# Optimization experiments

Measured on AMD Instinct MI355X. Metric: run time of the kernel, lower is better.

Reference implementation:

```python
import jax, jax.numpy as jnp
import numpy as np

D = 256      # input_dim (object feature dim)
H = 256      # hidden_dim
N0 = 4096    # nodes in frame 0
N1 = 4096    # nodes in frame 1
E = 131072   # edges
MP_ITER = 3
LN_EPS = 1e-5


def _glorot(k, shape):
    return jax.random.normal(k, shape, jnp.float32) * (1.0 / np.sqrt(shape[0]))


def setup_inputs() -> dict:
    key = jax.random.key(0)
    ks = jax.random.split(key, 20)
    z = lambda n: jnp.zeros((n,), jnp.float32)
    o = lambda n: jnp.ones((n,), jnp.float32)
    return {
        'node0': jax.random.normal(ks[0], (N0, D), jnp.float32),
        'node1': jax.random.normal(ks[1], (N1, D), jnp.float32),
        'row': jax.random.randint(ks[2], (E,), 0, N0, jnp.int32),
        'col': jax.random.randint(ks[3], (E,), 0, N1, jnp.int32),
        # edge_mlp: Linear(2D,H) ReLU Linear(H,H) LN ReLU Linear(H,H)
        'e_w1': _glorot(ks[4], (2 * D, H)), 'e_b1': z(H),
        'e_w2': _glorot(ks[5], (H, H)),     'e_b2': z(H),
        'e_g': o(H), 'e_be': z(H),
        'e_w3': _glorot(ks[6], (H, H)),     'e_b3': z(H),
        # node_mlp: Linear(H+D,H) ReLU Linear(H,H) LN ReLU Linear(H,D)
        'n_w1': _glorot(ks[7], (H + D, H)), 'n_b1': z(H),
        'n_w2': _glorot(ks[8], (H, H)),     'n_b2': z(H),
        'n_g': o(H), 'n_be': z(H),
        'n_w3': _glorot(ks[9], (H, D)),     'n_b3': z(D),
        # edge_predictor: Linear(2D,H) ReLU Linear(H,1)
        'p_w1': _glorot(ks[10], (2 * D, H)), 'p_b1': z(H),
        'p_w2': _glorot(ks[11], (H, 1)),     'p_b2': z(1),
    }


def _ln(x, g, b):
    mu = jnp.mean(x, axis=-1, keepdims=True)
    var = jnp.mean(jnp.square(x - mu), axis=-1, keepdims=True)
    return (x - mu) * jax.lax.rsqrt(var + LN_EPS) * g + b


def reference(node0, node1, row, col,
              e_w1, e_b1, e_w2, e_b2, e_g, e_be, e_w3, e_b3,
              n_w1, n_b1, n_w2, n_b2, n_g, n_be, n_w3, n_b3,
              p_w1, p_b1, p_w2, p_b2):
    def edge_mlp(x):
        h = jax.nn.relu(x @ e_w1 + e_b1)
        h = _ln(h @ e_w2 + e_b2, e_g, e_be)
        return jax.nn.relu(h) @ e_w3 + e_b3

    def node_mlp(x):
        h = jax.nn.relu(x @ n_w1 + n_b1)
        h = _ln(h @ n_w2 + n_b2, n_g, n_be)
        return jax.nn.relu(h) @ n_w3 + n_b3

    for _ in range(MP_ITER):
        # gather -> edge MLP -> scatter-add -> node MLP (+ residual)
        e_in = jnp.concatenate([node0[row], node1[col]], axis=1)  # [E, 2D]
        edge_attr = edge_mlp(e_in)                                 # [E, H]
        agg = jax.ops.segment_sum(edge_attr, row, num_segments=node0.shape[0])  # [N0, H]
        node0 = node_mlp(jnp.concatenate([node0, agg], axis=1)) + node0

    pred_in = jnp.concatenate([node0[row], node1[col]], axis=1)   # [E, 2D]
    h = jax.nn.relu(pred_in @ p_w1 + p_b1)
    edge_preds = jax.nn.sigmoid(h @ p_w2 + p_b2)                   # [E, 1]
    return edge_preds
```

## Files before the change

kernel.cpp:

```cpp
#include <hip/hip_runtime.h>
#include <hip/hip_bf16.h>

#define NN0 4096
#define NEDGE 131072
#define NMP 3

typedef __attribute__((ext_vector_type(8))) short bf16x8;
typedef __attribute__((ext_vector_type(4))) float f32x4;

__device__ __forceinline__ unsigned short f2b(float v) {
  __hip_bfloat16 h = __float2bfloat16(v);
  return __builtin_bit_cast(unsigned short, h);
}

__device__ __forceinline__ float b2f(short s) {
  return __builtin_bit_cast(float, ((unsigned)(unsigned short)s) << 16);
}

__device__ __forceinline__ void gload_lds16(const void* g, void* l) {
  __builtin_amdgcn_global_load_lds(
      (const __attribute__((address_space(1))) void*)g,
      (__attribute__((address_space(3))) void*)l, 16, 0, 0);
}

#define MFMA(a, b, c) __builtin_amdgcn_mfma_f32_16x16x32_bf16((a), (b), (c), 0, 0, 0)

__device__ __forceinline__ void wfrag_body(const float* __restrict__ src,
                                           unsigned short* __restrict__ dst,
                                           int t, int C, int lgnkt) {
  const int j = t & 7;
  const int l = (t >> 3) & 63;
  const int rest = t >> 9;
  const int kt = rest & ((1 << lgnkt) - 1);
  const int ct = rest >> lgnkt;
  const int r = l & 15, q = l >> 4;
  const int k = (kt << 5) + (q << 3) + j;
  const int c = (ct << 4) + r;
  dst[t] = f2b(src[k * C + c]);
}

__global__ void prep_kernel(
    const float* e1, const float* e2, const float* e3,
    const float* n1, const float* n2, const float* n3, const float* p1,
    unsigned short* We1, unsigned short* We2, unsigned short* We3,
    unsigned short* Wn1, unsigned short* Wn2, unsigned short* Wn3,
    unsigned short* Wp1,
    const float* __restrict__ node0, const float* __restrict__ node1,
    unsigned short* __restrict__ n0b, float* __restrict__ n0f,
    unsigned short* __restrict__ n1b,
    const int* __restrict__ rowi, int* __restrict__ counts) {
  const int b = blockIdx.x;
  const int tid = threadIdx.x;
  if (b < 512)       wfrag_body(e1, We1, (b - 0) * 256 + tid, 256, 4);
  else if (b < 768)  wfrag_body(e2, We2, (b - 512) * 256 + tid, 256, 3);
  else if (b < 1024) wfrag_body(e3, We3, (b - 768) * 256 + tid, 256, 3);
  else if (b < 1536) wfrag_body(n1, Wn1, (b - 1024) * 256 + tid, 256, 4);
  else if (b < 1792) wfrag_body(n2, Wn2, (b - 1536) * 256 + tid, 256, 3);
  else if (b < 2048) wfrag_body(n3, Wn3, (b - 1792) * 256 + tid, 256, 3);
  else if (b < 2560) wfrag_body(p1, Wp1, (b - 2048) * 256 + tid, 256, 4);
  else {
    const int t = (b - 2560) * 256 + tid;
    const float a = node0[t], v = node1[t];
    n0b[t] = f2b(a);
    n0f[t] = a;
    n1b[t] = f2b(v);
    if (t < NEDGE) atomicAdd(&counts[rowi[t]], 1);
  }
}

__global__ void scan_kernel(const int* __restrict__ counts, int* __restrict__ pos) {
  __shared__ int part[256];
  const int t = threadIdx.x;
  const int base = t << 4;
  int local[16];
  int s = 0;
  #pragma unroll
  for (int i = 0; i < 16; ++i) { local[i] = s; s += counts[base + i]; }
  part[t] = s;
  __syncthreads();
  int val = s;
  #pragma unroll
  for (int off = 1; off < 256; off <<= 1) {
    const int add = (t >= off) ? part[t - off] : 0;
    __syncthreads();
    val += add;
    part[t] = val;
    __syncthreads();
  }
  const int excl = val - s;
  #pragma unroll
  for (int i = 0; i < 16; ++i) pos[base + i] = excl + local[i];
}

__global__ void fill_kernel(const int* __restrict__ rowi, int* __restrict__ pos,
                            int* __restrict__ perm) {
  const int e = blockIdx.x * 256 + threadIdx.x;
  if (e < NEDGE) {
    const int slot = atomicAdd(&pos[rowi[e]], 1);
    perm[slot] = e;
  }
}

__global__ __launch_bounds__(256, 2) void pre_gemm_kernel(
    const unsigned short* __restrict__ n0bA, const unsigned short* __restrict__ n1b,
    const unsigned short* __restrict__ We1, const unsigned short* __restrict__ Wp1,
    const float* __restrict__ e_b1,
    unsigned short* __restrict__ P0, unsigned short* __restrict__ P1,
    unsigned short* __restrict__ Pp1)
{
  __shared__ unsigned short smem[32 * 256];
  const int b = blockIdx.x;
  const int grp = b >> 7, mb = b & 127;
  const unsigned short* A;
  const unsigned short* W;
  int ktoff;
  const float* bias;
  unsigned short* out;
  if (grp == 0)      { A = n0bA; W = We1; ktoff = 0; bias = e_b1;    out = P0;  }
  else if (grp == 1) { A = n1b;  W = We1; ktoff = 8; bias = nullptr; out = P1;  }
  else               { A = n1b;  W = Wp1; ktoff = 8; bias = nullptr; out = Pp1; }

  const int tid = (int)threadIdx.x;
  const int ww = tid >> 6, l = tid & 63, r = l & 15, q = l >> 4;
  const int c0 = ww << 6;
  const int swz = (r & 7) << 4;

  #pragma unroll
  for (int s = 0; s < 4; ++s) {
    const int rp = (ww << 3) + (s << 1);
    const int row = rp + (l >> 5);
    const int g = (l & 31) ^ (row & 7);
    gload_lds16(A + (mb * 32 + row) * 256 + g * 8, &smem[rp * 256]);
  }
  __syncthreads();

  f32x4 acc[2][4];
  #pragma unroll
  for (int mt = 0; mt < 2; ++mt)
    #pragma unroll
    for (int nt = 0; nt < 4; ++nt)
      acc[mt][nt] = f32x4{0.f, 0.f, 0.f, 0.f};

  for (int ks = 0; ks < 8; ++ks) {
    bf16x8 a[2];
    #pragma unroll
    for (int mt = 0; mt < 2; ++mt)
      a[mt] = *(const bf16x8*)((const char*)smem + ((mt << 4) + r) * 512 +
                               (((ks << 6) | (q << 4)) ^ swz));
    #pragma unroll
    for (int nt = 0; nt < 4; ++nt) {
      bf16x8 bfr = *(const bf16x8*)(W + ((((ww << 2) + nt) << 4) + ktoff + ks) * 512 + (l << 3));
      #pragma unroll
      for (int mt = 0; mt < 2; ++mt)
        acc[mt][nt] = MFMA(a[mt], bfr, acc[mt][nt]);
    }
  }
  #pragma unroll
  for (int nt = 0; nt < 4; ++nt) {
    const int col = c0 + (nt << 4) + r;
    const float bv = bias ? bias[col] : 0.f;
    #pragma unroll
    for (int mt = 0; mt < 2; ++mt)
      #pragma unroll
      for (int i = 0; i < 4; ++i)
        out[(mb * 32 + (mt << 4) + (q << 2) + i) * 256 + col] = f2b(acc[mt][nt][i] + bv);
  }
}

__global__ __launch_bounds__(512, 2) void edge_mlp_kernel(
    const unsigned short* __restrict__ P0b, const unsigned short* __restrict__ P1b,
    const int* __restrict__ rowi, const int* __restrict__ coli,
    const int* __restrict__ perm,
    const unsigned short* __restrict__ W2, const float* __restrict__ b2,
    const float* __restrict__ lng, const float* __restrict__ lnb,
    float* __restrict__ S)
{
  __shared__ unsigned short smem[128 * 256];
  __shared__ float lnp[1024];
  __shared__ int rs_s[128];
  __shared__ int cs_s[128];

  const int tid = (int)threadIdx.x;
  const int ww = tid >> 6, l = tid & 63, r = l & 15, q = l >> 4;
  const int wm = ww >> 2, wn = ww & 3;
  const int e0 = (int)blockIdx.x * 128;
  const int c0 = wn << 6;
  const int rbase = wm << 6;
  const int swz = (r & 7) << 4;

  const int hrow = tid >> 2;
  const int cq = tid & 3;
  const int pe = perm[e0 + hrow];
  const int mrow = rowi[pe], mcol = coli[pe];
  if (cq == 0) { rs_s[hrow] = mrow; cs_s[hrow] = mcol; }
  const unsigned short* pu = P0b + mrow * 256;
  const unsigned short* pv = P1b + mcol * 256;
  const int hswz = (hrow & 7) << 4;

  #pragma unroll
  for (int jb = 0; jb < 2; ++jb) {
    bf16x8 uu[4], vv[4];
    #pragma unroll
    for (int j = 0; j < 4; ++j) {
      const int col0 = (cq << 6) + (jb << 5) + (j << 3);
      uu[j] = *(const bf16x8*)(pu + col0);
      vv[j] = *(const bf16x8*)(pv + col0);
    }
    #pragma unroll
    for (int j = 0; j < 4; ++j) {
      const int col0 = (cq << 6) + (jb << 5) + (j << 3);
      bf16x8 hpk;
      #pragma unroll
      for (int k = 0; k < 8; ++k)
        hpk[k] = (short)f2b(fmaxf(b2f(uu[j][k]) + b2f(vv[j][k]), 0.f));
      *(bf16x8*)((char*)smem + hrow * 512 + (((unsigned)(col0 * 2)) ^ hswz)) = hpk;
    }
  }
  __syncthreads();

  f32x4 acc2[4][4];
  #pragma unroll
  for (int mt = 0; mt < 4; ++mt)
    #pragma unroll
    for (int nt = 0; nt < 4; ++nt)
      acc2[mt][nt] = f32x4{0.f, 0.f, 0.f, 0.f};
  __builtin_amdgcn_s_setprio(1);
  for (int ks = 0; ks < 8; ++ks) {
    bf16x8 a[4];
    #pragma unroll
    for (int mt = 0; mt < 4; ++mt)
      a[mt] = *(const bf16x8*)((const char*)smem + (rbase + (mt << 4) + r) * 512 +
                               (((ks << 6) | (q << 4)) ^ swz));
    #pragma unroll
    for (int nt = 0; nt < 4; ++nt) {
      bf16x8 b = *(const bf16x8*)(W2 + ((((wn << 2) + nt) << 3) + ks) * 512 + (l << 3));
      #pragma unroll
      for (int mt = 0; mt < 4; ++mt)
        acc2[mt][nt] = MFMA(a[mt], b, acc2[mt][nt]);
    }
  }
  __builtin_amdgcn_s_setprio(0);
  #pragma unroll
  for (int nt = 0; nt < 4; ++nt) {
    const float bias = b2[c0 + (nt << 4) + r];
    #pragma unroll
    for (int mt = 0; mt < 4; ++mt)
      #pragma unroll
      for (int i = 0; i < 4; ++i)
        acc2[mt][nt][i] += bias;
  }
  #pragma unroll
  for (int mt = 0; mt < 4; ++mt)
    #pragma unroll
    for (int i = 0; i < 4; ++i) {
      float s = 0.f, s2 = 0.f;
      #pragma unroll
      for (int nt = 0; nt < 4; ++nt) { const float x = acc2[mt][nt][i]; s += x; s2 += x * x; }
      #pragma unroll
      for (int m = 1; m < 16; m <<= 1) { s += __shfl_xor(s, m, 64); s2 += __shfl_xor(s2, m, 64); }
      if (r == 0) {
        const int rr = rbase + (mt << 4) + (q << 2) + i;
        lnp[wn * 128 + rr] = s;
        lnp[512 + wn * 128 + rr] = s2;
      }
    }
  __syncthreads();
  float mu[4][4], rstd[4][4];
  #pragma unroll
  for (int mt = 0; mt < 4; ++mt)
    #pragma unroll
    for (int i = 0; i < 4; ++i) {
      const int rr = rbase + (mt << 4) + (q << 2) + i;
      const float s  = lnp[rr] + lnp[128 + rr] + lnp[256 + rr] + lnp[384 + rr];
      const float s2 = lnp[512 + rr] + lnp[512 + 128 + rr] + lnp[512 + 256 + rr] + lnp[512 + 384 + rr];
      const float mean = s * (1.f / 256.f);
      const float var = s2 * (1.f / 256.f) - mean * mean;
      mu[mt][i] = mean;
      rstd[mt][i] = rsqrtf(var + 1e-5f);
    }
  #pragma unroll
  for (int nt = 0; nt < 4; ++nt) {
    const int hc = c0 + (nt << 4) + r;
    const float gv = lng[hc], bv = lnb[hc];
    #pragma unroll
    for (int mt = 0; mt < 4; ++mt)
      #pragma unroll
      for (int i = 0; i < 4; ++i) {
        const int hr = rbase + (mt << 4) + (q << 2) + i;
        const float x = fmaxf((acc2[mt][nt][i] - mu[mt][i]) * rstd[mt][i] * gv + bv, 0.f);
        *(unsigned short*)((char*)smem + hr * 512 + ((hc * 2) ^ ((hr & 7) << 4))) = f2b(x);
      }
  }
  __syncthreads();

  const int cp = tid & 127;
  const int seg = tid >> 7;
  float s0 = 0.f, s1 = 0.f;
  #pragma unroll
  for (int j = 0; j < 32; ++j) {
    const int er = (seg << 5) + j;
    const unsigned v = *(const unsigned*)((const char*)smem + er * 512 +
                                          ((cp << 2) ^ ((er & 7) << 4)));
    s0 += b2f((short)(v & 0xffffu));
    s1 += b2f((short)(v >> 16));
    if ((j == 31) || (rs_s[er] != rs_s[er + 1])) {
      float* dst = S + rs_s[er] * 256 + (cp << 1);
      atomicAdd(dst, s0);
      atomicAdd(dst + 1, s1);
      s0 = 0.f; s1 = 0.f;
    }
  }
}

__global__ __launch_bounds__(512, 2) void node_mlp_kernel(
    float* __restrict__ nf, float* __restrict__ S, const int* __restrict__ counts,
    const unsigned short* __restrict__ W1, const float* __restrict__ b1,
    const unsigned short* __restrict__ W2, const float* __restrict__ b2,
    const float* __restrict__ lng, const float* __restrict__ lnb,
    const unsigned short* __restrict__ W3, const float* __restrict__ b3,
    const unsigned short* __restrict__ We3, const float* __restrict__ e_b3,
    const unsigned short* __restrict__ We1, const float* __restrict__ e_b1,
    const unsigned short* __restrict__ Wp1, const float* __restrict__ p_b1,
    unsigned short* __restrict__ P0out, unsigned short* __restrict__ Pp0out)
{
  __shared__ unsigned short smem[16 * 512];
  __shared__ unsigned short Slds[16 * 256];
  __shared__ float lnp[256];
  const int tid = (int)threadIdx.x;
  const int ww = tid >> 6, l = tid & 63, r = l & 15, q = l >> 4;
  const int r0 = (int)blockIdx.x << 4;
  const int c0 = ww << 5;
  const int swz = (r & 7) << 4;

  {
    const int arow = tid >> 5;
    const int kc = tid & 31;
    const int nrow = r0 + arow;
    const int sw = (arow & 7) << 4;
    float v[16];
    if (kc < 16) {
      const float* src = nf + nrow * 256 + (kc << 4);
      *(f32x4*)(v + 0)  = *(const f32x4*)(src + 0);
      *(f32x4*)(v + 4)  = *(const f32x4*)(src + 4);
      *(f32x4*)(v + 8)  = *(const f32x4*)(src + 8);
      *(f32x4*)(v + 12) = *(const f32x4*)(src + 12);
      bf16x8 p0, p1;
      #pragma unroll
      for (int k = 0; k < 8; ++k) { p0[k] = (short)f2b(v[k]); p1[k] = (short)f2b(v[8 + k]); }
      const int base = arow * 1024;
      const int b0 = kc << 5;
      *(bf16x8*)((char*)smem + base + (b0 ^ sw)) = p0;
      *(bf16x8*)((char*)smem + base + ((b0 + 16) ^ sw)) = p1;
    } else {
      const int kc2 = kc - 16;
      float* src = S + nrow * 256 + (kc2 << 4);
      *(f32x4*)(v + 0)  = *(const f32x4*)(src + 0);
      *(f32x4*)(v + 4)  = *(const f32x4*)(src + 4);
      *(f32x4*)(v + 8)  = *(const f32x4*)(src + 8);
      *(f32x4*)(v + 12) = *(const f32x4*)(src + 12);
      *(f32x4*)(src + 0) = f32x4{0.f, 0.f, 0.f, 0.f};
      *(f32x4*)(src + 4) = f32x4{0.f, 0.f, 0.f, 0.f};
      *(f32x4*)(src + 8) = f32x4{0.f, 0.f, 0.f, 0.f};
      *(f32x4*)(src + 12) = f32x4{0.f, 0.f, 0.f, 0.f};
      bf16x8 p0, p1;
      #pragma unroll
      for (int k = 0; k < 8; ++k) { p0[k] = (short)f2b(v[k]); p1[k] = (short)f2b(v[8 + k]); }
      const int base = arow * 512;
      const int b0 = kc2 << 5;
      *(bf16x8*)((char*)Slds + base + (b0 ^ sw)) = p0;
      *(bf16x8*)((char*)Slds + base + ((b0 + 16) ^ sw)) = p1;
    }
  }
  __syncthreads();

  {
    f32x4 acc0[2];
    acc0[0] = f32x4{0.f, 0.f, 0.f, 0.f};
    acc0[1] = f32x4{0.f, 0.f, 0.f, 0.f};
    for (int ks = 0; ks < 8; ++ks) {
      bf16x8 a = *(const bf16x8*)((const char*)Slds + r * 512 + (((ks << 6) | (q << 4)) ^ swz));
      #pragma unroll
      for (int nt = 0; nt < 2; ++nt) {
        bf16x8 b = *(const bf16x8*)(We3 + ((((ww << 1) + nt) << 3) + ks) * 512 + (l << 3));
        acc0[nt] = MFMA(a, b, acc0[nt]);
      }
    }
    float degv[4];
    #pragma unroll
    for (int i = 0; i < 4; ++i) degv[i] = (float)counts[r0 + (q << 2) + i];
    #pragma unroll
    for (int nt = 0; nt < 2; ++nt) {
      const int col = c0 + (nt << 4) + r;
      const float bv = e_b3[col];
      #pragma unroll
      for (int i = 0; i < 4; ++i) {
        const int arow = (q << 2) + i;
        const float vv = acc0[nt][i] + degv[i] * bv;
        *(unsigned short*)((char*)smem + arow * 1024 +
                           (((512 + (col << 1))) ^ ((arow & 7) << 4))) = f2b(vv);
      }
    }
  }
  __syncthreads();

  f32x4 acc1[2];
  acc1[0] = f32x4{0.f, 0.f, 0.f, 0.f};
  acc1[1] = f32x4{0.f, 0.f, 0.f, 0.f};
  for (int ks = 0; ks < 16; ++ks) {
    bf16x8 a = *(const bf16x8*)((const char*)smem + r * 1024 + (((ks << 6) | (q << 4)) ^ swz));
    #pragma unroll
    for (int nt = 0; nt < 2; ++nt) {
      bf16x8 b = *(const bf16x8*)(W1 + ((((ww << 1) + nt) << 4) + ks) * 512 + (l << 3));
      acc1[nt] = MFMA(a, b, acc1[nt]);
    }
  }
  #pragma unroll
  for (int nt = 0; nt < 2; ++nt) {
    const float bias = b1[c0 + (nt << 4) + r];
    #pragma unroll
    for (int i = 0; i < 4; ++i) acc1[nt][i] = fmaxf(acc1[nt][i] + bias, 0.f);
  }
  __syncthreads();
  #pragma unroll
  for (int i = 0; i < 4; ++i) {
    const int hr = (q << 2) + i;
    const int hswz2 = (hr & 7) << 4;
    #pragma unroll
    for (int nt = 0; nt < 2; ++nt) {
      const int hc = c0 + (nt << 4) + r;
      *(unsigned short*)((char*)smem + hr * 512 + ((hc * 2) ^ hswz2)) = f2b(acc1[nt][i]);
    }
  }
  __syncthreads();

  f32x4 acc2[2];
  acc2[0] = f32x4{0.f, 0.f, 0.f, 0.f};
  acc2[1] = f32x4{0.f, 0.f, 0.f, 0.f};
  for (int ks = 0; ks < 8; ++ks) {
    bf16x8 a = *(const bf16x8*)((const char*)smem + r * 512 + (((ks << 6) | (q << 4)) ^ swz));
    #pragma unroll
    for (int nt = 0; nt < 2; ++nt) {
      bf16x8 b = *(const bf16x8*)(W2 + ((((ww << 1) + nt) << 3) + ks) * 512 + (l << 3));
      acc2[nt] = MFMA(a, b, acc2[nt]);
    }
  }
  #pragma unroll
  for (int nt = 0; nt < 2; ++nt) {
    const float bias = b2[c0 + (nt << 4) + r];
    #pragma unroll
    for (int i = 0; i < 4; ++i) acc2[nt][i] += bias;
  }
  #pragma unroll
  for (int i = 0; i < 4; ++i) {
    float s = acc2[0][i] + acc2[1][i];
    float s2 = acc2[0][i] * acc2[0][i] + acc2[1][i] * acc2[1][i];
    #pragma unroll
    for (int m = 1; m < 16; m <<= 1) { s += __shfl_xor(s, m, 64); s2 += __shfl_xor(s2, m, 64); }
    if (r == 0) {
      const int rr = (q << 2) + i;
      lnp[ww * 16 + rr] = s;
      lnp[128 + ww * 16 + rr] = s2;
    }
  }
  __syncthreads();
  float mu[4], rstd[4];
  #pragma unroll
  for (int i = 0; i < 4; ++i) {
    const int rr = (q << 2) + i;
    float s = 0.f, s2 = 0.f;
    #pragma unroll
    for (int w2i = 0; w2i < 8; ++w2i) { s += lnp[w2i * 16 + rr]; s2 += lnp[128 + w2i * 16 + rr]; }
    const float mean = s * (1.f / 256.f);
    const float var = s2 * (1.f / 256.f) - mean * mean;
    mu[i] = mean;
    rstd[i] = rsqrtf(var + 1e-5f);
  }
  #pragma unroll
  for (int nt = 0; nt < 2; ++nt) {
    const int hc = c0 + (nt << 4) + r;
    const float gv = lng[hc], bv = lnb[hc];
    #pragma unroll
    for (int i = 0; i < 4; ++i) {
      const int hr = (q << 2) + i;
      const float x = fmaxf((acc2[nt][i] - mu[i]) * rstd[i] * gv + bv, 0.f);
      *(unsigned short*)((char*)smem + hr * 512 + ((hc * 2) ^ ((hr & 7) << 4))) = f2b(x);
    }
  }
  __syncthreads();

  f32x4 acc3[2];
  acc3[0] = f32x4{0.f, 0.f, 0.f, 0.f};
  acc3[1] = f32x4{0.f, 0.f, 0.f, 0.f};
  for (int ks = 0; ks < 8; ++ks) {
    bf16x8 a = *(const bf16x8*)((const char*)smem + r * 512 + (((ks << 6) | (q << 4)) ^ swz));
    #pragma unroll
    for (int nt = 0; nt < 2; ++nt) {
      bf16x8 b = *(const bf16x8*)(W3 + ((((ww << 1) + nt) << 3) + ks) * 512 + (l << 3));
      acc3[nt] = MFMA(a, b, acc3[nt]);
    }
  }
  float y_loc[4][2];
  #pragma unroll
  for (int nt = 0; nt < 2; ++nt) {
    const float bias3 = b3[c0 + (nt << 4) + r];
    #pragma unroll
    for (int i = 0; i < 4; ++i) {
      const int nrow = r0 + (q << 2) + i;
      const int col = c0 + (nt << 4) + r;
      const float y = acc3[nt][i] + bias3 + nf[nrow * 256 + col];
      nf[nrow * 256 + col] = y;
      y_loc[i][nt] = y;
    }
  }
  __syncthreads();
  #pragma unroll
  for (int i = 0; i < 4; ++i) {
    const int hr = (q << 2) + i;
    const int hswz2 = (hr & 7) << 4;
    #pragma unroll
    for (int nt = 0; nt < 2; ++nt) {
      const int hc = c0 + (nt << 4) + r;
      *(unsigned short*)((char*)smem + hr * 512 + ((hc * 2) ^ hswz2)) = f2b(y_loc[i][nt]);
    }
  }
  __syncthreads();

  f32x4 acc4[2];
  acc4[0] = f32x4{0.f, 0.f, 0.f, 0.f};
  acc4[1] = f32x4{0.f, 0.f, 0.f, 0.f};
  for (int ks = 0; ks < 8; ++ks) {
    bf16x8 a = *(const bf16x8*)((const char*)smem + r * 512 + (((ks << 6) | (q << 4)) ^ swz));
    #pragma unroll
    for (int nt = 0; nt < 2; ++nt) {
      bf16x8 b = *(const bf16x8*)(We1 + ((((ww << 1) + nt) << 4) + ks) * 512 + (l << 3));
      acc4[nt] = MFMA(a, b, acc4[nt]);
    }
  }
  #pragma unroll
  for (int nt = 0; nt < 2; ++nt) {
    const int col = c0 + (nt << 4) + r;
    const float bv = e_b1[col];
    #pragma unroll
    for (int i = 0; i < 4; ++i)
      P0out[(r0 + (q << 2) + i) * 256 + col] = f2b(acc4[nt][i] + bv);
  }

  if (Pp0out != nullptr) {
    f32x4 acc5[2];
    acc5[0] = f32x4{0.f, 0.f, 0.f, 0.f};
    acc5[1] = f32x4{0.f, 0.f, 0.f, 0.f};
    for (int ks = 0; ks < 8; ++ks) {
      bf16x8 a = *(const bf16x8*)((const char*)smem + r * 512 + (((ks << 6) | (q << 4)) ^ swz));
      #pragma unroll
      for (int nt = 0; nt < 2; ++nt) {
        bf16x8 b = *(const bf16x8*)(Wp1 + ((((ww << 1) + nt) << 4) + ks) * 512 + (l << 3));
        acc5[nt] = MFMA(a, b, acc5[nt]);
      }
    }
    #pragma unroll
    for (int nt = 0; nt < 2; ++nt) {
      const int col = c0 + (nt << 4) + r;
      const float bv = p_b1[col];
      #pragma unroll
      for (int i = 0; i < 4; ++i)
        Pp0out[(r0 + (q << 2) + i) * 256 + col] = f2b(acc5[nt][i] + bv);
    }
  }
}

__global__ __launch_bounds__(256, 4) void pred_kernel(
    const unsigned short* __restrict__ Pp0, const unsigned short* __restrict__ Pp1,
    const int* __restrict__ rowi, const int* __restrict__ coli,
    const int* __restrict__ perm,
    const float* __restrict__ w2, const float* __restrict__ b2,
    float* __restrict__ out)
{
  const int g = (int)blockIdx.x * 256 + (int)threadIdx.x;
  const int e = perm[g];
  const int prow = rowi[e] * 256, pcol = coli[e] * 256;
  float acc = 0.f;
  #pragma unroll 4
  for (int j = 0; j < 32; ++j) {
    const bf16x8 u = *(const bf16x8*)(Pp0 + prow + (j << 3));
    const bf16x8 v = *(const bf16x8*)(Pp1 + pcol + (j << 3));
    #pragma unroll
    for (int k = 0; k < 8; ++k)
      acc += fmaxf(b2f(u[k]) + b2f(v[k]), 0.f) * w2[(j << 3) + k];
  }
  out[e] = 1.f / (1.f + expf(-(acc + b2[0])));
}

extern "C" void kernel_launch(void* const* d_in, const int* in_sizes, int n_in,
                              void* d_out, int out_size, void* d_ws, size_t ws_size,
                              hipStream_t stream) {
  const float* node0 = (const float*)d_in[0];
  const float* node1 = (const float*)d_in[1];
  const int* rowi = (const int*)d_in[2];
  const int* coli = (const int*)d_in[3];
  const float* e_w1 = (const float*)d_in[4];
  const float* e_b1 = (const float*)d_in[5];
  const float* e_w2 = (const float*)d_in[6];
  const float* e_b2 = (const float*)d_in[7];
  const float* e_g  = (const float*)d_in[8];
  const float* e_be = (const float*)d_in[9];
  const float* e_w3 = (const float*)d_in[10];
  const float* e_b3 = (const float*)d_in[11];
  const float* n_w1 = (const float*)d_in[12];
  const float* n_b1 = (const float*)d_in[13];
  const float* n_w2 = (const float*)d_in[14];
  const float* n_b2 = (const float*)d_in[15];
  const float* n_g  = (const float*)d_in[16];
  const float* n_be = (const float*)d_in[17];
  const float* n_w3 = (const float*)d_in[18];
  const float* n_b3 = (const float*)d_in[19];
  const float* p_w1 = (const float*)d_in[20];
  const float* p_b1 = (const float*)d_in[21];
  const float* p_w2 = (const float*)d_in[22];
  const float* p_b2 = (const float*)d_in[23];

  char* ws = (char*)d_ws;
  unsigned short* WTe1 = (unsigned short*)(ws + 0);
  unsigned short* WTe2 = (unsigned short*)(ws + 262144);
  unsigned short* WTe3 = (unsigned short*)(ws + 393216);
  unsigned short* WTn1 = (unsigned short*)(ws + 524288);
  unsigned short* WTn2 = (unsigned short*)(ws + 786432);
  unsigned short* WTn3 = (unsigned short*)(ws + 917504);
  unsigned short* WTp1 = (unsigned short*)(ws + 1048576);
  unsigned short* n1b  = (unsigned short*)(ws + 1310720);
  unsigned short* n0b  = (unsigned short*)(ws + 3407872);
  unsigned short* P0b  = (unsigned short*)(ws + 5505024);
  unsigned short* P1b  = (unsigned short*)(ws + 7602176);
  unsigned short* Pp0b = (unsigned short*)(ws + 9699328);
  unsigned short* Pp1b = (unsigned short*)(ws + 11796480);
  float* n0f  = (float*)(ws + 13893632);
  float* agg  = (float*)(ws + 18087936);
  int* perm   = (int*)(ws + 22282240);
  int* posb   = (int*)(ws + 22806528);
  int* counts = (int*)(ws + 22822912);

  hipMemsetAsync(counts, 0, 4096 * 4, stream);
  hipMemsetAsync(agg, 0, (size_t)NN0 * 256 * 4, stream);
  prep_kernel<<<6656, 256, 0, stream>>>(e_w1, e_w2, e_w3, n_w1, n_w2, n_w3, p_w1,
                                        WTe1, WTe2, WTe3, WTn1, WTn2, WTn3, WTp1,
                                        node0, node1, n0b, n0f, n1b, rowi, counts);
  scan_kernel<<<1, 256, 0, stream>>>(counts, posb);
  fill_kernel<<<512, 256, 0, stream>>>(rowi, posb, perm);

  pre_gemm_kernel<<<384, 256, 0, stream>>>(n0b, n1b, WTe1, WTp1, e_b1, P0b, P1b, Pp1b);

  for (int it = 0; it < NMP; ++it) {
    edge_mlp_kernel<<<NEDGE / 128, 512, 0, stream>>>(P0b, P1b, rowi, coli, perm,
        WTe2, e_b2, e_g, e_be, agg);
    node_mlp_kernel<<<NN0 / 16, 512, 0, stream>>>(n0f, agg, counts,
        WTn1, n_b1, WTn2, n_b2, n_g, n_be, WTn3, n_b3,
        WTe3, e_b3, WTe1, e_b1, WTp1, p_b1, P0b, (it == NMP - 1) ? Pp0b : nullptr);
  }
  pred_kernel<<<NEDGE / 256, 256, 0, stream>>>(Pp0b, Pp1b, rowi, coli, perm,
      p_w2, p_b2, (float*)d_out);
}
```

Baseline: 330.4 us.

## Restructure edge MLP so each wave owns 16 full edge rows

The edge MLP kernel is reorganised so that each wavefront handles 16 edges across all 256 output columns. The gathered relu(u+v) inputs feed straight into MFMA registers, with no block-wide LDS staging. LayerNorm statistics are reduced inside the wave, which removes the cross-wave LDS partial sums and all block barriers. Segment boundaries for the scatter-add are found with a ballot. The trade-off is that each wave must load the full W2 slice per edge tile, so B-operand traffic per edge rises, and the wave holds 16 accumulators. Atomic segments are also shorter (16 rows instead of 32), which may increase atomic count.

```diff
diff --git a/kernel.cpp b/kernel.cpp
--- a/kernel.cpp
+++ b/kernel.cpp
@@ -167,7 +167,7 @@
   }
 }
 
-__global__ __launch_bounds__(512, 2) void edge_mlp_kernel(
+__global__ __launch_bounds__(256, 4) void edge_mlp_kernel(
     const unsigned short* __restrict__ P0b, const unsigned short* __restrict__ P1b,
     const int* __restrict__ rowi, const int* __restrict__ coli,
     const int* __restrict__ perm,
@@ -175,139 +175,96 @@
     const float* __restrict__ lng, const float* __restrict__ lnb,
     float* __restrict__ S)
 {
-  __shared__ unsigned short smem[128 * 256];
-  __shared__ float lnp[1024];
-  __shared__ int rs_s[128];
-  __shared__ int cs_s[128];
+  __shared__ unsigned short smem[4][16 * 256];
+  __shared__ int rs_w[4][16];
 
   const int tid = (int)threadIdx.x;
-  const int ww = tid >> 6, l = tid & 63, r = l & 15, q = l >> 4;
-  const int wm = ww >> 2, wn = ww & 3;
-  const int e0 = (int)blockIdx.x * 128;
-  const int c0 = wn << 6;
-  const int rbase = wm << 6;
-  const int swz = (r & 7) << 4;
-
-  const int hrow = tid >> 2;
-  const int cq = tid & 3;
-  const int pe = perm[e0 + hrow];
-  const int mrow = rowi[pe], mcol = coli[pe];
-  if (cq == 0) { rs_s[hrow] = mrow; cs_s[hrow] = mcol; }
-  const unsigned short* pu = P0b + mrow * 256;
-  const unsigned short* pv = P1b + mcol * 256;
-  const int hswz = (hrow & 7) << 4;
-
-  #pragma unroll
-  for (int jb = 0; jb < 2; ++jb) {
-    bf16x8 uu[4], vv[4];
-    #pragma unroll
-    for (int j = 0; j < 4; ++j) {
-      const int col0 = (cq << 6) + (jb << 5) + (j << 3);
-      uu[j] = *(const bf16x8*)(pu + col0);
-      vv[j] = *(const bf16x8*)(pv + col0);
-    }
-    #pragma unroll
-    for (int j = 0; j < 4; ++j) {
-      const int col0 = (cq << 6) + (jb << 5) + (j << 3);
-      bf16x8 hpk;
-      #pragma unroll
-      for (int k = 0; k < 8; ++k)
-        hpk[k] = (short)f2b(fmaxf(b2f(uu[j][k]) + b2f(vv[j][k]), 0.f));
-      *(bf16x8*)((char*)smem + hrow * 512 + (((unsigned)(col0 * 2)) ^ hswz)) = hpk;
-    }
-  }
-  __syncthreads();
-
-  f32x4 acc2[4][4];
-  #pragma unroll
-  for (int mt = 0; mt < 4; ++mt)
-    #pragma unroll
-    for (int nt = 0; nt < 4; ++nt)
-      acc2[mt][nt] = f32x4{0.f, 0.f, 0.f, 0.f};
-  __builtin_amdgcn_s_setprio(1);
+  const int w = tid >> 6, l = tid & 63, r = l & 15, q = l >> 4;
+  const int e0 = (int)blockIdx.x * 64 + (w << 4);
+
+  const int pe = perm[e0 + r];
+  const int mrow = rowi[pe];
+  const int mcol = coli[pe];
+  if (l < 16) rs_w[w][l] = mrow;
+  const unsigned short* pu = P0b + mrow * 256 + (q << 3);
+  const unsigned short* pv = P1b + mcol * 256 + (q << 3);
+
+  unsigned long long bm;
+  {
+    const int nxt = __shfl(mrow, r + 1);
+    const bool bnd = (l < 16) && ((l == 15) || (mrow != nxt));
+    bm = __ballot(bnd) & 0xffffull;
+  }
+
+  f32x4 acc[16];
+  #pragma unroll
+  for (int ct = 0; ct < 16; ++ct) acc[ct] = f32x4{0.f, 0.f, 0.f, 0.f};
   for (int ks = 0; ks < 8; ++ks) {
-    bf16x8 a[4];
-    #pragma unroll
-    for (int mt = 0; mt < 4; ++mt)
-      a[mt] = *(const bf16x8*)((const char*)smem + (rbase + (mt << 4) + r) * 512 +
-                               (((ks << 6) | (q << 4)) ^ swz));
-    #pragma unroll
-    for (int nt = 0; nt < 4; ++nt) {
-      bf16x8 b = *(const bf16x8*)(W2 + ((((wn << 2) + nt) << 3) + ks) * 512 + (l << 3));
-      #pragma unroll
-      for (int mt = 0; mt < 4; ++mt)
-        acc2[mt][nt] = MFMA(a[mt], b, acc2[mt][nt]);
-    }
-  }
-  __builtin_amdgcn_s_setprio(0);
-  #pragma unroll
-  for (int nt = 0; nt < 4; ++nt) {
-    const float bias = b2[c0 + (nt << 4) + r];
-    #pragma unroll
-    for (int mt = 0; mt < 4; ++mt)
-      #pragma unroll
-      for (int i = 0; i < 4; ++i)
-        acc2[mt][nt][i] += bias;
-  }
-  #pragma unroll
-  for (int mt = 0; mt < 4; ++mt)
+    const bf16x8 uu = *(const bf16x8*)(pu + (ks << 5));
+    const bf16x8 vv = *(const bf16x8*)(pv + (ks << 5));
+    bf16x8 a;
+    #pragma unroll
+    for (int k = 0; k < 8; ++k)
+      a[k] = (short)f2b(fmaxf(b2f(uu[k]) + b2f(vv[k]), 0.f));
+    __builtin_amdgcn_s_setprio(1);
+    #pragma unroll
+    for (int ct = 0; ct < 16; ++ct) {
+      bf16x8 b = *(const bf16x8*)(W2 + (((ct << 3) + ks) << 9) + (l << 3));
+      acc[ct] = MFMA(a, b, acc[ct]);
+    }
+    __builtin_amdgcn_s_setprio(0);
+  }
+
+  #pragma unroll
+  for (int ct = 0; ct < 16; ++ct) {
+    const float bv = b2[(ct << 4) + r];
+    #pragma unroll
+    for (int i = 0; i < 4; ++i) acc[ct][i] += bv;
+  }
+
+  float mu[4], rstd[4];
+  #pragma unroll
+  for (int i = 0; i < 4; ++i) {
+    float s = 0.f, s2 = 0.f;
+    #pragma unroll
+    for (int ct = 0; ct < 16; ++ct) { const float x = acc[ct][i]; s += x; s2 += x * x; }
+    #pragma unroll
+    for (int m = 1; m < 16; m <<= 1) { s += __shfl_xor(s, m, 64); s2 += __shfl_xor(s2, m, 64); }
+    const float mean = s * (1.f / 256.f);
+    const float var = s2 * (1.f / 256.f) - mean * mean;
+    mu[i] = mean;
+    rstd[i] = rsqrtf(var + 1e-5f);
+  }
+
+  unsigned short* hl = smem[w];
+  #pragma unroll
+  for (int ct = 0; ct < 16; ++ct) {
+    const int col = (ct << 4) + r;
+    const float gv = lng[col], bv = lnb[col];
     #pragma unroll
     for (int i = 0; i < 4; ++i) {
-      float s = 0.f, s2 = 0.f;
-      #pragma unroll
-      for (int nt = 0; nt < 4; ++nt) { const float x = acc2[mt][nt][i]; s += x; s2 += x * x; }
-      #pragma unroll
-      for (int m = 1; m < 16; m <<= 1) { s += __shfl_xor(s, m, 64); s2 += __shfl_xor(s2, m, 64); }
-      if (r == 0) {
-        const int rr = rbase + (mt << 4) + (q << 2) + i;
-        lnp[wn * 128 + rr] = s;
-        lnp[512 + wn * 128 + rr] = s2;
+      const int row = (q << 2) + i;
+      const float x = fmaxf((acc[ct][i] - mu[i]) * rstd[i] * gv + bv, 0.f);
+      *(unsigned short*)((char*)hl + row * 512 + ((col * 2) ^ ((row & 7) << 4))) = f2b(x);
+    }
+  }
+
+  #pragma unroll
+  for (int cc = 0; cc < 2; ++cc) {
+    const int cp = (cc << 6) + l;
+    float s0 = 0.f, s1 = 0.f;
+    #pragma unroll
+    for (int j = 0; j < 16; ++j) {
+      const unsigned v = *(const unsigned*)((const char*)hl + j * 512 +
+                                            ((cp << 2) ^ ((j & 7) << 4)));
+      s0 += b2f((short)(v & 0xffffu));
+      s1 += b2f((short)(v >> 16));
+      if ((bm >> j) & 1ull) {
+        float* dst = S + rs_w[w][j] * 256 + (cp << 1);
+        atomicAdd(dst, s0);
+        atomicAdd(dst + 1, s1);
+        s0 = 0.f; s1 = 0.f;
       }
-    }
-  __syncthreads();
-  float mu[4][4], rstd[4][4];
-  #pragma unroll
-  for (int mt = 0; mt < 4; ++mt)
-    #pragma unroll
-    for (int i = 0; i < 4; ++i) {
-      const int rr = rbase + (mt << 4) + (q << 2) + i;
-      const float s  = lnp[rr] + lnp[128 + rr] + lnp[256 + rr] + lnp[384 + rr];
-      const float s2 = lnp[512 + rr] + lnp[512 + 128 + rr] + lnp[512 + 256 + rr] + lnp[512 + 384 + rr];
-      const float mean = s * (1.f / 256.f);
-      const float var = s2 * (1.f / 256.f) - mean * mean;
-      mu[mt][i] = mean;
-      rstd[mt][i] = rsqrtf(var + 1e-5f);
-    }
-  #pragma unroll
-  for (int nt = 0; nt < 4; ++nt) {
-    const int hc = c0 + (nt << 4) + r;
-    const float gv = lng[hc], bv = lnb[hc];
-    #pragma unroll
-    for (int mt = 0; mt < 4; ++mt)
-      #pragma unroll
-      for (int i = 0; i < 4; ++i) {
-        const int hr = rbase + (mt << 4) + (q << 2) + i;
-        const float x = fmaxf((acc2[mt][nt][i] - mu[mt][i]) * rstd[mt][i] * gv + bv, 0.f);
-        *(unsigned short*)((char*)smem + hr * 512 + ((hc * 2) ^ ((hr & 7) << 4))) = f2b(x);
-      }
-  }
-  __syncthreads();
-
-  const int cp = tid & 127;
-  const int seg = tid >> 7;
-  float s0 = 0.f, s1 = 0.f;
-  #pragma unroll
-  for (int j = 0; j < 32; ++j) {
-    const int er = (seg << 5) + j;
-    const unsigned v = *(const unsigned*)((const char*)smem + er * 512 +
-                                          ((cp << 2) ^ ((er & 7) << 4)));
-    s0 += b2f((short)(v & 0xffffu));
-    s1 += b2f((short)(v >> 16));
-    if ((j == 31) || (rs_s[er] != rs_s[er + 1])) {
-      float* dst = S + rs_s[er] * 256 + (cp << 1);
-      atomicAdd(dst, s0);
-      atomicAdd(dst + 1, s1);
-      s0 = 0.f; s1 = 0.f;
     }
   }
 }
@@ -649,7 +606,7 @@
   pre_gemm_kernel<<<384, 256, 0, stream>>>(n0b, n1b, WTe1, WTp1, e_b1, P0b, P1b, Pp1b);
 
   for (int it = 0; it < NMP; ++it) {
-    edge_mlp_kernel<<<NEDGE / 128, 512, 0, stream>>>(P0b, P1b, rowi, coli, perm,
+    edge_mlp_kernel<<<NEDGE / 64, 256, 0, stream>>>(P0b, P1b, rowi, coli, perm,
         WTe2, e_b2, e_g, e_be, agg);
     node_mlp_kernel<<<NN0 / 16, 512, 0, stream>>>(n0f, agg, counts,
         WTn1, n_b1, WTn2, n_b2, n_g, n_be, WTn3, n_b3,
```

Result: slower. 386.5 us (+17.0%).
